# Optimization experiments

Hardware: AMD Instinct MI355X
Metric: run time of the kernel (lower is better)

The kernel has to match this reference:

```python
import jax, jax.numpy as jnp
import numpy as np

IN_DIM = 128
OUT_DIM = 128
NUM_RELS = 8
N_NODES = 50000
N_EDGES = 500000


def setup_inputs() -> dict:
    key = jax.random.key(0)
    k_x, k_ei_s, k_ei_d, k_et, k_w, k_sw = jax.random.split(key, 6)
    x = jax.random.normal(k_x, (N_NODES, IN_DIM), dtype=jnp.float32)
    src = jax.random.randint(k_ei_s, (N_EDGES,), 0, N_NODES)
    dst = jax.random.randint(k_ei_d, (N_EDGES,), 0, N_NODES)
    edge_index = jnp.stack([src, dst], axis=0).astype(jnp.int64)
    edge_type = jax.random.randint(k_et, (N_EDGES,), 0, NUM_RELS).astype(jnp.int64)
    # xavier_uniform: bound = sqrt(6/(fan_in+fan_out))
    bw = float(np.sqrt(6.0 / (IN_DIM + OUT_DIM)))
    weight = jax.random.uniform(k_w, (NUM_RELS, IN_DIM, OUT_DIM), dtype=jnp.float32, minval=-bw, maxval=bw)
    self_loop_weight = jax.random.uniform(k_sw, (IN_DIM, OUT_DIM), dtype=jnp.float32, minval=-bw, maxval=bw)
    bias = jnp.zeros((OUT_DIM,), dtype=jnp.float32)
    return {
        "x": x,
        "weight": weight,
        "self_loop_weight": self_loop_weight,
        "bias": bias,
        "edge_index": edge_index,
        "edge_type": edge_type,
        "num_entities": N_NODES,
    }


def reference(x, weight, self_loop_weight, bias, edge_index, edge_type, num_entities):
    # Relation-grouped formulation of the per-edge loop:
    # transform every node under every relation once: hr[r, n, o]
    hr = jnp.einsum("nd,rdo->rno", x, weight)
    src, dst = edge_index[0], edge_index[1]
    # per-edge message = x[src] @ weight[edge_type]  == hr[edge_type, src]
    msg = hr[edge_type, src]  # [E, out]
    agg = jax.ops.segment_sum(msg, dst, num_segments=num_entities)  # scatter-add into out[dst]
    out = agg + x @ self_loop_weight + bias
    return jax.nn.relu(out)
```

## Files before the change

### kernel.cpp

```cpp
#include <hip/hip_runtime.h>

#define IN_DIM 128
#define OUT_DIM 128
#define NUM_RELS 8

typedef unsigned short u16;
typedef u16 u16x8 __attribute__((ext_vector_type(8)));
typedef u16 u16x4 __attribute__((ext_vector_type(4)));
typedef __bf16 bf16x8 __attribute__((ext_vector_type(8)));
typedef float f32x4 __attribute__((ext_vector_type(4)));

__device__ __forceinline__ u16 f2bf(float f) {
    unsigned u = __float_as_uint(f);
    u += 0x7FFF + ((u >> 16) & 1);
    return (u16)(u >> 16);
}
__device__ __forceinline__ float bf2f(u16 h) {
    return __uint_as_float((unsigned)h << 16);
}

__global__ __launch_bounds__(256) void k_zero(int4* __restrict__ p, int n4)
{
    int i = blockIdx.x * 256 + threadIdx.x;
    if (i < n4) p[i] = make_int4(0, 0, 0, 0);
}

__global__ __launch_bounds__(256) void k_prep(
    const float* __restrict__ x, const float* __restrict__ weight,
    const float* __restrict__ slw,
    const int* __restrict__ dst, const int* __restrict__ et,
    u16* __restrict__ xb, u16* __restrict__ WbT, int* __restrict__ cursor,
    int* __restrict__ row_ptr,
    int N, int E, int n8, int BA, int BB)
{
    const int b = blockIdx.x;
    const int tid = threadIdx.x;
    if (b == 0 && tid == 0) row_ptr[n8] = E;
    if (b < BA) {
        long i = ((long)b * 256 + tid) * 4;
        if (i < (long)N * 128) {
            float4 v = *(const float4*)(x + i);
            u16x4 o;
            o[0] = f2bf(v.x); o[1] = f2bf(v.y); o[2] = f2bf(v.z); o[3] = f2bf(v.w);
            *(u16x4*)(xb + i) = o;
        }
    } else if (b < BA + BB) {
        int i = ((b - BA) * 256 + tid) * 4;
        if (i < 128 * 1152) {
            const int col = i / 1152;
            const int kk  = i - col * 1152;
            u16x4 o;
            #pragma unroll
            for (int j = 0; j < 4; ++j) {
                const int kj = kk + j;
                const float f = (kj < 1024)
                    ? weight[((kj >> 7) << 14) + ((kj & 127) << 7) + col]
                    : slw[((kj - 1024) << 7) + col];
                o[j] = f2bf(f);
            }
            *(u16x4*)(WbT + i) = o;
        }
    } else {
        int e = (b - BA - BB) * 256 + tid;
        if (e < E) atomicAdd(&cursor[(dst[e] << 3) + et[e]], 1);
    }
}

__global__ __launch_bounds__(512) void k_scan_lb(
    const int* __restrict__ deg, int* __restrict__ row_ptr,
    int* __restrict__ cursor, unsigned long long* __restrict__ part, int n)
{
    __shared__ int s[512];
    __shared__ int s_exc;
    const int c = blockIdx.x;
    const int t = threadIdx.x;
    const int base = (c << 12) + (t << 3);
    int v[8]; int sum = 0;
    #pragma unroll
    for (int j = 0; j < 8; ++j) {
        const int i = base + j;
        v[j] = (i < n) ? deg[i] : 0;
        sum += v[j];
    }
    s[t] = sum;
    __syncthreads();
    #pragma unroll
    for (int off = 1; off < 512; off <<= 1) {
        const int y = (t >= off) ? s[t - off] : 0;
        __syncthreads();
        s[t] += y;
        __syncthreads();
    }
    const int total = s[511];
    const int run = s[t] - sum;

    if (t == 0) {
        const unsigned long long st = (c == 0) ? 2ULL : 1ULL;
        __hip_atomic_store(&part[c], (st << 32) | (unsigned int)total,
                           __ATOMIC_RELAXED, __HIP_MEMORY_SCOPE_AGENT);
    }

    int exc = 0;
    if (c > 0 && t < 64) {
        int bj = c - 1;
        while (true) {
            const int idx = bj - t;
            unsigned long long w = 0;
            if (idx >= 0) {
                do {
                    w = __hip_atomic_load(&part[idx], __ATOMIC_RELAXED,
                                          __HIP_MEMORY_SCOPE_AGENT);
                } while ((w >> 32) == 0ULL);
            }
            const unsigned long long incmask =
                __ballot(idx >= 0 && (w >> 32) == 2ULL);
            const int Ls = incmask ? (__ffsll(incmask) - 1) : 64;
            unsigned int contrib =
                (idx >= 0 && t <= Ls) ? (unsigned int)(w & 0xffffffffULL) : 0u;
            #pragma unroll
            for (int o = 32; o >= 1; o >>= 1) contrib += __shfl_xor(contrib, o);
            exc += (int)contrib;
            if (Ls < 64) break;
            bj -= 64;
        }
        if (t == 0) {
            __hip_atomic_store(&part[c],
                (2ULL << 32) | (unsigned int)(exc + total),
                __ATOMIC_RELAXED, __HIP_MEMORY_SCOPE_AGENT);
            s_exc = exc;
        }
    } else if (t == 0) {
        s_exc = 0;
    }
    __syncthreads();
    exc = s_exc;
    int acc_ = exc + run;
    #pragma unroll
    for (int j = 0; j < 8; ++j) {
        const int i = base + j;
        if (i < n) { row_ptr[i] = acc_; cursor[i] = acc_; }
        acc_ += v[j];
    }
}

__global__ __launch_bounds__(256) void k_fill(
    const int* __restrict__ src, const int* __restrict__ dst,
    const int* __restrict__ et, int* __restrict__ cursor,
    int* __restrict__ packed, int E)
{
    int e = blockIdx.x * blockDim.x + threadIdx.x;
    if (e >= E) return;
    int pos = atomicAdd(&cursor[(dst[e] << 3) + et[e]], 1);
    packed[pos] = (et[e] << 17) | src[e];
}

#define NPB 64
#define LDK 392

__device__ __forceinline__ void gather8(
    u16* arow, const u16* __restrict__ xb, const int* __restrict__ packed,
    int beg, int end, int r0, int r1, int lo)
{
    float a[16];
    #pragma unroll
    for (int j = 0; j < 16; ++j) a[j] = 0.f;
    int cur = r0;

    auto flush = [&]() {
        u16x8 ol, oh;
        #pragma unroll
        for (int j = 0; j < 8; ++j) {
            ol[j] = f2bf(a[j]);     a[j] = 0.f;
            oh[j] = f2bf(a[8 + j]); a[8 + j] = 0.f;
        }
        u16* p = arow + ((cur - r0) << 7) + lo;
        *(u16x8*)p = ol;
        *(u16x8*)(p + 8) = oh;
        ++cur;
    };
    auto proc = [&](int p, const u16x8& vl, const u16x8& vh) {
        const int r_ = p >> 17;
        while (cur < r_) flush();
        #pragma unroll
        for (int j = 0; j < 8; ++j) {
            a[j]     += bf2f(vl[j]);
            a[8 + j] += bf2f(vh[j]);
        }
    };

    int k = beg;
    for (; k + 4 <= end; k += 4) {
        const int p0 = packed[k],     p1 = packed[k + 1];
        const int p2 = packed[k + 2], p3 = packed[k + 3];
        const u16* b0 = xb + ((size_t)(p0 & 0x1FFFF) << 7) + lo;
        const u16* b1 = xb + ((size_t)(p1 & 0x1FFFF) << 7) + lo;
        const u16* b2 = xb + ((size_t)(p2 & 0x1FFFF) << 7) + lo;
        const u16* b3 = xb + ((size_t)(p3 & 0x1FFFF) << 7) + lo;
        const u16x8 v0l = *(const u16x8*)b0, v0h = *(const u16x8*)(b0 + 8);
        const u16x8 v1l = *(const u16x8*)b1, v1h = *(const u16x8*)(b1 + 8);
        const u16x8 v2l = *(const u16x8*)b2, v2h = *(const u16x8*)(b2 + 8);
        const u16x8 v3l = *(const u16x8*)b3, v3h = *(const u16x8*)(b3 + 8);
        proc(p0, v0l, v0h); proc(p1, v1l, v1h);
        proc(p2, v2l, v2h); proc(p3, v3l, v3h);
    }
    for (; k < end; ++k) {
        const int p = packed[k];
        const u16* b = xb + ((size_t)(p & 0x1FFFF) << 7) + lo;
        const u16x8 vl = *(const u16x8*)b, vh = *(const u16x8*)(b + 8);
        proc(p, vl, vh);
    }
    while (cur < r1) flush();
}

__global__ __launch_bounds__(512, 6) void fused_rgcn(
    const u16* __restrict__ xb,
    const u16* __restrict__ WbT,
    const float* __restrict__ bias,
    const int* __restrict__ row_ptr,
    const int* __restrict__ packed,
    float* __restrict__ out, int N)
{
    __shared__ u16 agg[NPB][LDK];

    const int tid = threadIdx.x;
    const int n0 = blockIdx.x * NPB;
    const int lane = tid & 63;
    const int wv = tid >> 6;
    const int q = lane >> 4, l = lane & 15;
    const int cbase = wv << 4;
    const int grp = tid >> 3;
    const int lo  = (tid & 7) << 4;
    const int gn = n0 + grp;
    u16* arow = &agg[grp][0];
    const float bv = bias[cbase + l];

    f32x4 acc[4] = {};

    #pragma unroll 1
    for (int ck = 0; ck < 3; ++ck) {
        const int r0 = ck * 3;
        const int r1 = (ck == 2) ? 8 : r0 + 3;

        if (gn < N) {
            const int beg = row_ptr[(gn << 3) + r0];
            const int end = row_ptr[(gn << 3) + r1];
            gather8(arow, xb, packed, beg, end, r0, r1, lo);
            if (ck == 2) {
                const u16* sb = xb + ((size_t)gn << 7) + lo;
                *(u16x8*)(arow + 256 + lo)     = *(const u16x8*)sb;
                *(u16x8*)(arow + 256 + lo + 8) = *(const u16x8*)(sb + 8);
            }
        }
        __syncthreads();

        const u16* Bp = WbT + (size_t)(cbase + l) * 1152 + ck * 384 + (q << 3);
        #pragma unroll
        for (int kk = 0; kk < 12; ++kk) {
            const int k0 = (kk << 5) + (q << 3);
            const bf16x8 b = __builtin_bit_cast(bf16x8, *(const u16x8*)(Bp + (kk << 5)));
            #pragma unroll
            for (int mt = 0; mt < 4; ++mt) {
                const bf16x8 a = __builtin_bit_cast(
                    bf16x8, *(const u16x8*)(&agg[(mt << 4) + l][k0]));
                acc[mt] = __builtin_amdgcn_mfma_f32_16x16x32_bf16(a, b, acc[mt], 0, 0, 0);
            }
        }
        if (ck < 2) __syncthreads();
    }

    #pragma unroll
    for (int mt = 0; mt < 4; ++mt) {
        const int rbase = n0 + (mt << 4) + (q << 2);
        #pragma unroll
        for (int j = 0; j < 4; ++j) {
            const int row = rbase + j;
            if (row < N)
                out[(size_t)row * 128 + cbase + l] = fmaxf(acc[mt][j] + bv, 0.f);
        }
    }
}

__global__ __launch_bounds__(256) void gemm128(
    const float* __restrict__ x, const float* __restrict__ W,
    const float* __restrict__ bias, float* __restrict__ out, int N)
{
    __shared__ float Ws[IN_DIM * OUT_DIM];
    __shared__ float xs[16][IN_DIM];

    const float* Wz = W + (size_t)blockIdx.z * IN_DIM * OUT_DIM;
    float* outz = out + (size_t)blockIdx.z * (size_t)N * OUT_DIM;

    {
        const float4* s4 = (const float4*)Wz;
        float4* d4 = (float4*)Ws;
        for (int i = threadIdx.x; i < IN_DIM * OUT_DIM / 4; i += 256)
            d4[i] = s4[i];
    }

    const int tid = threadIdx.x;
    const int nl = (tid >> 5) * 2;
    const int og = (tid & 31) * 4;

    float4 b4 = make_float4(0.f, 0.f, 0.f, 0.f);
    if (bias) b4 = *(const float4*)&bias[og];

    const int nchunks = (N + 15) / 16;
    for (int chunk = blockIdx.x; chunk < nchunks; chunk += gridDim.x) {
        const int n0 = chunk * 16;
        const int rows = min(16, N - n0);
        __syncthreads();
        {
            const float4* xsrc = (const float4*)(x + (size_t)n0 * IN_DIM);
            float4* xdst = (float4*)&xs[0][0];
            const int n4 = rows * (IN_DIM / 4);
            for (int i = tid; i < n4; i += 256) xdst[i] = xsrc[i];
        }
        __syncthreads();

        if (nl < rows) {
            float a00 = 0.f, a01 = 0.f, a02 = 0.f, a03 = 0.f;
            float a10 = 0.f, a11 = 0.f, a12 = 0.f, a13 = 0.f;
            #pragma unroll 8
            for (int d = 0; d < IN_DIM; ++d) {
                const float4 w4 = *(const float4*)&Ws[d * OUT_DIM + og];
                const float xa = xs[nl][d];
                const float xb = xs[nl + 1][d];
                a00 += xa * w4.x; a01 += xa * w4.y; a02 += xa * w4.z; a03 += xa * w4.w;
                a10 += xb * w4.x; a11 += xb * w4.y; a12 += xb * w4.z; a13 += xb * w4.w;
            }
            float4 r0 = make_float4(a00 + b4.x, a01 + b4.y, a02 + b4.z, a03 + b4.w);
            *(float4*)&outz[(size_t)(n0 + nl) * OUT_DIM + og] = r0;
            if (nl + 1 < rows) {
                float4 r1 = make_float4(a10 + b4.x, a11 + b4.y, a12 + b4.z, a13 + b4.w);
                *(float4*)&outz[(size_t)(n0 + nl + 1) * OUT_DIM + og] = r1;
            }
        }
    }
}

__global__ __launch_bounds__(256) void edge_direct(
    const float* __restrict__ x, const float* __restrict__ W,
    const int* __restrict__ src, const int* __restrict__ dst,
    const int* __restrict__ et, float* __restrict__ out, int E)
{
    long t = (long)blockIdx.x * blockDim.x + threadIdx.x;
    long e = t >> 6;
    int lane = (int)(t & 63);
    if (e >= E) return;
    int s = src[e], d = dst[e], r = et[e];
    const float* xr = x + (long)s * IN_DIM;
    float2 xv = *(const float2*)(xr + lane * 2);
    const float* Wr = W + (long)r * IN_DIM * OUT_DIM;
    const int o0 = lane * 2;
    float a0 = 0.f, a1 = 0.f;
    #pragma unroll 8
    for (int dd = 0; dd < 64; ++dd) {
        float xa = __shfl(xv.x, dd);
        float xb = __shfl(xv.y, dd);
        a0 += xa * Wr[(2 * dd) * OUT_DIM + o0]     + xb * Wr[(2 * dd + 1) * OUT_DIM + o0];
        a1 += xa * Wr[(2 * dd) * OUT_DIM + o0 + 1] + xb * Wr[(2 * dd + 1) * OUT_DIM + o0 + 1];
    }
    atomicAdd(out + (long)d * OUT_DIM + o0, a0);
    atomicAdd(out + (long)d * OUT_DIM + o0 + 1, a1);
}

__global__ __launch_bounds__(256) void relu_k(float* __restrict__ out, long n4)
{
    long i = (long)blockIdx.x * blockDim.x + threadIdx.x;
    if (i >= n4) return;
    float4 v = ((float4*)out)[i];
    v.x = fmaxf(v.x, 0.f); v.y = fmaxf(v.y, 0.f);
    v.z = fmaxf(v.z, 0.f); v.w = fmaxf(v.w, 0.f);
    ((float4*)out)[i] = v;
}

static inline size_t align256(size_t x) { return (x + 255) & ~(size_t)255; }

extern "C" void kernel_launch(void* const* d_in, const int* in_sizes, int n_in,
                              void* d_out, int out_size, void* d_ws, size_t ws_size,
                              hipStream_t stream)
{
    const float* x      = (const float*)d_in[0];
    const float* weight = (const float*)d_in[1];
    const float* slw    = (const float*)d_in[2];
    const float* bias   = (const float*)d_in[3];
    const int*   ei     = (const int*)d_in[4];
    const int*   et     = (const int*)d_in[5];

    const int N = in_sizes[0] / IN_DIM;
    const int E = in_sizes[5];
    const int* src  = ei;
    const int* dstp = ei + E;

    float* out = (float*)d_out;

    const int n8 = N * 8;

    size_t off = 0;
    const size_t xb_off   = off; off += align256((size_t)N * 128 * 2);
    const size_t wb_off   = off; off += align256((size_t)128 * 1152 * 2);
    const size_t rp_off   = off; off += align256((size_t)(n8 + 1) * 4);
    const size_t cur_off  = off; off += align256((size_t)n8 * 4);
    const size_t pt_off   = off; off += align256(256 * 8);
    const size_t pk_off   = off; off += align256((size_t)E * 4);
    const size_t need_bf16 = off;

    const int nchunks = (n8 + 4095) >> 12;

    if (ws_size >= need_bf16 && N <= (1 << 17) && nchunks <= 256) {
        char* base   = (char*)d_ws;
        u16* xb      = (u16*)(base + xb_off);
        u16* WbT     = (u16*)(base + wb_off);
        int* row_ptr = (int*)(base + rp_off);
        int* cursor  = (int*)(base + cur_off);
        unsigned long long* part = (unsigned long long*)(base + pt_off);
        int* packed  = (int*)(base + pk_off);

        const int n4z = (int)((pk_off - cur_off) / 16);
        k_zero<<<dim3((n4z + 255) / 256), 256, 0, stream>>>(
            (int4*)(base + cur_off), n4z);

        const int BA = (int)(((long)N * 128 / 4 + 255) / 256);
        const int BB = (128 * 1152 / 4 + 255) / 256;
        const int BD = (E + 255) / 256;
        k_prep<<<dim3(BA + BB + BD), 256, 0, stream>>>(
            x, weight, slw, dstp, et, xb, WbT, cursor, row_ptr, N, E, n8, BA, BB);

        k_scan_lb<<<dim3(nchunks), 512, 0, stream>>>(cursor, row_ptr, cursor, part, n8);
        k_fill<<<dim3((E + 255) / 256), 256, 0, stream>>>(src, dstp, et, cursor, packed, E);

        const int ntiles = (N + NPB - 1) / NPB;
        fused_rgcn<<<dim3(ntiles), 512, 0, stream>>>(
            xb, WbT, bias, row_ptr, packed, out, N);
    } else if (ws_size >= (size_t)NUM_RELS * N * 128 * 4) {
        gemm128<<<dim3(512, 1, 1), 256, 0, stream>>>(x, slw, bias, out, N);
        long nt = (long)E * 64;
        edge_direct<<<dim3((nt + 255) / 256), 256, 0, stream>>>(x, weight, src, dstp, et, out, E);
        long n4 = (long)N * OUT_DIM / 4;
        relu_k<<<dim3((n4 + 255) / 256), 256, 0, stream>>>(out, n4);
    } else {
        gemm128<<<dim3(512, 1, 1), 256, 0, stream>>>(x, slw, bias, out, N);
        long nt = (long)E * 64;
        edge_direct<<<dim3((nt + 255) / 256), 256, 0, stream>>>(x, weight, src, dstp, et, out, E);
        long n4 = (long)N * OUT_DIM / 4;
        relu_k<<<dim3((n4 + 255) / 256), 256, 0, stream>>>(out, n4);
    }
}
```

Baseline: 227.7 us.

## Split fused gather+GEMM into separate gather kernel and MFMA GEMM kernel

```diff
diff --git a/kernel.cpp b/kernel.cpp
--- a/kernel.cpp
+++ b/kernel.cpp
@@ -154,6 +154,115 @@
     packed[pos] = (et[e] << 17) | src[e];
 }
 
+__global__ __launch_bounds__(256, 8) void k_gather(
+    const u16* __restrict__ xb,
+    const int* __restrict__ row_ptr,
+    const int* __restrict__ packed,
+    u16* __restrict__ agg,
+    int N)
+{
+    const int grp = threadIdx.x >> 4;
+    const int lo  = (threadIdx.x & 15) << 3;
+    const int gn  = blockIdx.x * 16 + grp;
+    if (gn >= N) return;
+
+    const int beg = row_ptr[gn << 3];
+    const int end = row_ptr[(gn << 3) + 8];
+    u16* arow = agg + (size_t)gn * 1152 + lo;
+
+    float a0=0.f,a1=0.f,a2=0.f,a3=0.f,a4=0.f,a5=0.f,a6=0.f,a7=0.f;
+    int cur = 0;
+
+#define FLUSH_() { u16x8 o_; \
+    o_[0]=f2bf(a0); o_[1]=f2bf(a1); o_[2]=f2bf(a2); o_[3]=f2bf(a3); \
+    o_[4]=f2bf(a4); o_[5]=f2bf(a5); o_[6]=f2bf(a6); o_[7]=f2bf(a7); \
+    *(u16x8*)(arow + (cur << 7)) = o_; \
+    a0=0.f;a1=0.f;a2=0.f;a3=0.f;a4=0.f;a5=0.f;a6=0.f;a7=0.f; ++cur; }
+
+#define PROC_(p_, v_) { const int r_ = (p_) >> 17; \
+    while (cur < r_) { FLUSH_(); } \
+    a0 += bf2f((v_)[0]); a1 += bf2f((v_)[1]); a2 += bf2f((v_)[2]); a3 += bf2f((v_)[3]); \
+    a4 += bf2f((v_)[4]); a5 += bf2f((v_)[5]); a6 += bf2f((v_)[6]); a7 += bf2f((v_)[7]); }
+
+    int k = beg;
+    for (; k + 8 <= end; k += 8) {
+        const int p0 = packed[k],     p1 = packed[k + 1];
+        const int p2 = packed[k + 2], p3 = packed[k + 3];
+        const int p4 = packed[k + 4], p5 = packed[k + 5];
+        const int p6 = packed[k + 6], p7 = packed[k + 7];
+        const u16x8 v0 = *(const u16x8*)(xb + ((size_t)(p0 & 0x1FFFF) << 7) + lo);
+        const u16x8 v1 = *(const u16x8*)(xb + ((size_t)(p1 & 0x1FFFF) << 7) + lo);
+        const u16x8 v2 = *(const u16x8*)(xb + ((size_t)(p2 & 0x1FFFF) << 7) + lo);
+        const u16x8 v3 = *(const u16x8*)(xb + ((size_t)(p3 & 0x1FFFF) << 7) + lo);
+        const u16x8 v4 = *(const u16x8*)(xb + ((size_t)(p4 & 0x1FFFF) << 7) + lo);
+        const u16x8 v5 = *(const u16x8*)(xb + ((size_t)(p5 & 0x1FFFF) << 7) + lo);
+        const u16x8 v6 = *(const u16x8*)(xb + ((size_t)(p6 & 0x1FFFF) << 7) + lo);
+        const u16x8 v7 = *(const u16x8*)(xb + ((size_t)(p7 & 0x1FFFF) << 7) + lo);
+        PROC_(p0, v0); PROC_(p1, v1); PROC_(p2, v2); PROC_(p3, v3);
+        PROC_(p4, v4); PROC_(p5, v5); PROC_(p6, v6); PROC_(p7, v7);
+    }
+    for (; k + 4 <= end; k += 4) {
+        const int p0 = packed[k],     p1 = packed[k + 1];
+        const int p2 = packed[k + 2], p3 = packed[k + 3];
+        const u16x8 v0 = *(const u16x8*)(xb + ((size_t)(p0 & 0x1FFFF) << 7) + lo);
+        const u16x8 v1 = *(const u16x8*)(xb + ((size_t)(p1 & 0x1FFFF) << 7) + lo);
+        const u16x8 v2 = *(const u16x8*)(xb + ((size_t)(p2 & 0x1FFFF) << 7) + lo);
+        const u16x8 v3 = *(const u16x8*)(xb + ((size_t)(p3 & 0x1FFFF) << 7) + lo);
+        PROC_(p0, v0); PROC_(p1, v1); PROC_(p2, v2); PROC_(p3, v3);
+    }
+    for (; k < end; ++k) {
+        const int p = packed[k];
+        const u16x8 v = *(const u16x8*)(xb + ((size_t)(p & 0x1FFFF) << 7) + lo);
+        PROC_(p, v);
+    }
+    while (cur < 8) { FLUSH_(); }
+#undef PROC_
+#undef FLUSH_
+
+    *(u16x8*)(arow + 1024) = *(const u16x8*)(xb + ((size_t)gn << 7) + lo);
+}
+
+__global__ __launch_bounds__(512, 6) void k_gemm(
+    const u16* __restrict__ agg,
+    const u16* __restrict__ WbT,
+    const float* __restrict__ bias,
+    float* __restrict__ out, int N)
+{
+    const int tid = threadIdx.x;
+    const int lane = tid & 63, wv = tid >> 6;
+    const int q = lane >> 4, l = lane & 15;
+    const int cbase = wv << 4;
+    const int n0 = blockIdx.x * 64;
+    const float bv = bias[cbase + l];
+
+    const u16* Bp = WbT + (size_t)(cbase + l) * 1152 + (q << 3);
+    const u16* Ap = agg + (size_t)(n0 + l) * 1152 + (q << 3);
+
+    f32x4 acc[4] = {};
+    #pragma unroll 4
+    for (int kk = 0; kk < 36; ++kk) {
+        const int ko = kk << 5;
+        const bf16x8 b = __builtin_bit_cast(bf16x8, *(const u16x8*)(Bp + ko));
+        #pragma unroll
+        for (int mt = 0; mt < 4; ++mt) {
+            const bf16x8 a = __builtin_bit_cast(
+                bf16x8, *(const u16x8*)(Ap + (size_t)mt * 16 * 1152 + ko));
+            acc[mt] = __builtin_amdgcn_mfma_f32_16x16x32_bf16(a, b, acc[mt], 0, 0, 0);
+        }
+    }
+
+    #pragma unroll
+    for (int mt = 0; mt < 4; ++mt) {
+        const int rbase = n0 + (mt << 4) + (q << 2);
+        #pragma unroll
+        for (int j = 0; j < 4; ++j) {
+            const int row = rbase + j;
+            if (row < N)
+                out[(size_t)row * 128 + cbase + l] = fmaxf(acc[mt][j] + bv, 0.f);
+        }
+    }
+}
+
 #define NPB 64
 #define LDK 392
 
@@ -213,11 +322,9 @@
 }
 
 __global__ __launch_bounds__(512, 6) void fused_rgcn(
-    const u16* __restrict__ xb,
-    const u16* __restrict__ WbT,
+    const u16* __restrict__ xb, const u16* __restrict__ WbT,
     const float* __restrict__ bias,
-    const int* __restrict__ row_ptr,
-    const int* __restrict__ packed,
+    const int* __restrict__ row_ptr, const int* __restrict__ packed,
     float* __restrict__ out, int N)
 {
     __shared__ u16 agg[NPB][LDK];
@@ -395,6 +502,7 @@
     float* out = (float*)d_out;
 
     const int n8 = N * 8;
+    const int ntiles64 = (N + 63) / 64;
 
     size_t off = 0;
     const size_t xb_off   = off; off += align256((size_t)N * 128 * 2);
@@ -403,11 +511,13 @@
     const size_t cur_off  = off; off += align256((size_t)n8 * 4);
     const size_t pt_off   = off; off += align256(256 * 8);
     const size_t pk_off   = off; off += align256((size_t)E * 4);
-    const size_t need_bf16 = off;
+    const size_t need_core = off;
+    const size_t ag_off   = off; off += align256((size_t)ntiles64 * 64 * 1152 * 2);
+    const size_t need_split = off;
 
     const int nchunks = (n8 + 4095) >> 12;
 
-    if (ws_size >= need_bf16 && N <= (1 << 17) && nchunks <= 256) {
+    if (ws_size >= need_core && N <= (1 << 17) && nchunks <= 256) {
         char* base   = (char*)d_ws;
         u16* xb      = (u16*)(base + xb_off);
         u16* WbT     = (u16*)(base + wb_off);
@@ -429,9 +539,15 @@
         k_scan_lb<<<dim3(nchunks), 512, 0, stream>>>(cursor, row_ptr, cursor, part, n8);
         k_fill<<<dim3((E + 255) / 256), 256, 0, stream>>>(src, dstp, et, cursor, packed, E);
 
-        const int ntiles = (N + NPB - 1) / NPB;
-        fused_rgcn<<<dim3(ntiles), 512, 0, stream>>>(
-            xb, WbT, bias, row_ptr, packed, out, N);
+        if (ws_size >= need_split) {
+            u16* agg = (u16*)(base + ag_off);
+            k_gather<<<dim3((N + 15) / 16), 256, 0, stream>>>(
+                xb, row_ptr, packed, agg, N);
+            k_gemm<<<dim3(ntiles64), 512, 0, stream>>>(agg, WbT, bias, out, N);
+        } else {
+            fused_rgcn<<<dim3((N + NPB - 1) / NPB), 512, 0, stream>>>(
+                xb, WbT, bias, row_ptr, packed, out, N);
+        }
     } else if (ws_size >= (size_t)NUM_RELS * N * 128 * 4) {
         gemm128<<<dim3(512, 1, 1), 256, 0, stream>>>(x, slw, bias, out, N);
         long nt = (long)E * 64;
```

Result: slower. 353.3 us (+55.2%).
